# Kernel tuning notes

Measured on AMD Instinct MI355X. Metric: run time of the kernel, lower is better.

## Reference

```python
import jax, jax.numpy as jnp
import numpy as np

N, C, T, V = 64, 64, 64, 25   # batch, channels, frames, joints
S, W = 8, 3                   # num_subset, window_size
IC = C // S                   # inter_channels = out_channels // num_subset = 8
OC = 64                       # out_channels
EPS = 1e-5


def setup_inputs() -> dict:
    key = jax.random.key(0)
    ks = jax.random.split(key, 24)
    std = 0.05
    x = jax.random.normal(ks[0], (N, C, V, T), jnp.float32)
    # fixed skeleton graphs (buffers, non-trainable)
    graph = (jax.random.uniform(ks[1], (S, V, V)) > 0.7).astype(jnp.float32)
    graph = jnp.clip(graph + jnp.eye(V, dtype=jnp.float32)[None], 0.0, 1.0)
    graph_a = jax.random.uniform(ks[2], (V, V), jnp.float32) / V
    # conv1x1 weights (out, in) + biases
    in_w = jax.random.normal(ks[3], (S * IC, C), jnp.float32) * std
    in_b = jax.random.normal(ks[4], (S * IC,), jnp.float32) * 0.01
    inup_w = jax.random.normal(ks[5], (S * IC, C), jnp.float32) * std
    inup_b = jax.random.normal(ks[6], (S * IC,), jnp.float32) * 0.01
    diff_w = jax.random.normal(ks[7], (C, C), jnp.float32) * std
    diff_b = jax.random.normal(ks[8], (C,), jnp.float32) * 0.01
    att0 = jnp.ones((1, S, W * V, V), jnp.float32) / V  # attention0s
    out_w = jax.random.normal(ks[9], (OC, S * C), jnp.float32) * std
    out_b = jax.random.normal(ks[10], (OC,), jnp.float32) * 0.01
    out_gamma = jnp.ones((OC,), jnp.float32)
    out_beta = jnp.zeros((OC,), jnp.float32)
    out_rm = jax.random.normal(ks[11], (OC,), jnp.float32) * 0.01
    out_rv = jnp.ones((OC,), jnp.float32)
    ff_w = jax.random.normal(ks[12], (OC, OC), jnp.float32) * std
    ff_b = jax.random.normal(ks[13], (OC,), jnp.float32) * 0.01
    ff_gamma = jnp.ones((OC,), jnp.float32)
    ff_beta = jnp.zeros((OC,), jnp.float32)
    ff_rm = jax.random.normal(ks[14], (OC,), jnp.float32) * 0.01
    ff_rv = jnp.ones((OC,), jnp.float32)
    return dict(x=x, graph=graph, graph_a=graph_a, in_w=in_w, in_b=in_b,
                inup_w=inup_w, inup_b=inup_b, diff_w=diff_w, diff_b=diff_b,
                att0=att0, out_w=out_w, out_b=out_b, out_gamma=out_gamma,
                out_beta=out_beta, out_rm=out_rm, out_rv=out_rv, ff_w=ff_w,
                ff_b=ff_b, ff_gamma=ff_gamma, ff_beta=ff_beta, ff_rm=ff_rm,
                ff_rv=ff_rv)


def _bn(x, g, b, m, v):  # inference-mode BatchNorm2d over channel dim 1
    scale = (g / jnp.sqrt(v + EPS))[None, :, None, None]
    return x * scale + (b - m * g / jnp.sqrt(v + EPS))[None, :, None, None]


def _leaky(x):
    return jnp.where(x > 0, x, 0.1 * x)


def _forward(x, graph, graph_a, in_w, in_b, inup_w, inup_b, diff_w, diff_b,
             att0, out_w, out_b, out_gamma, out_beta, out_rm, out_rv,
             ff_w, ff_b, ff_gamma, ff_beta, ff_rm, ff_rv):
    xp = jnp.transpose(x, (0, 1, 3, 2))          # (N,C,T,V)
    identity = xp
    # temporal window unfold: (N,C,T,W*V)
    xpad = jnp.pad(xp, ((0, 0), (0, 0), (1, 1), (0, 0)))
    upf = jnp.stack([xpad[:, :, w:w + T, :] for w in range(W)], axis=3)
    upf = upf.reshape(N, C, T, W * V)
    # q/k projections (conv1x1)
    k = (jnp.einsum('nctv,oc->notv', xp, in_w) + in_b[None, :, None, None])
    k = k.reshape(N, S, IC, T, V)
    q = (jnp.einsum('nctu,oc->notu', upf, inup_w) + inup_b[None, :, None, None])
    q = q.reshape(N, S, IC, T, W * V)
    att = jnp.einsum('nsctu,nsctv->nsuv', q, k) / (IC * T)  # (N,S,WV,V)
    # per-subset adjacency mask (graph[i] tiled over window rows)
    mask = jnp.tile(graph, (1, W, 1)) > 0                    # (S,WV,V)
    att = jnp.where(mask[None], att, jnp.float32(-9e15))
    att = jax.nn.softmax(att, axis=-1)
    # diff gate
    d = jnp.einsum('nctu,uv->nctv', xp, graph_a)
    d = jnp.einsum('nctv,oc->notv', d, diff_w) + diff_b[None, :, None, None]
    d = jnp.tile(d, (1, 1, 1, W)) - upf                      # (N,C,T,WV)
    d = d.reshape(N, S, C // S, T, W, V)
    gate = jax.nn.sigmoid(d.mean(axis=(2, 3, 5)))            # (N,S,W)
    att = att * jnp.tile(gate[..., None], (1, 1, V, 1))      # (N,S,WV,1) tiled
    att = att + att0
    # aggregate
    y = jnp.einsum('nctu,nsuv->nsctv', upf, att).reshape(N, S * C, T, V)
    y = _bn(jnp.einsum('nctv,oc->notv', y, out_w) + out_b[None, :, None, None],
            out_gamma, out_beta, out_rm, out_rv)
    y = _leaky(xp + y)                                       # downs1 = identity
    y = _bn(jnp.einsum('nctv,oc->notv', y, ff_w) + ff_b[None, :, None, None],
            ff_gamma, ff_beta, ff_rm, ff_rv)
    y = _leaky(xp + y)                                       # downs2 = identity
    z = jax.nn.relu(y + identity)
    return jnp.transpose(z, (0, 1, 3, 2))                    # back to (N,C,V,T)


def reference(x, graph, graph_a, in_w, in_b, inup_w, inup_b, diff_w, diff_b,
              att0, out_w, out_b, out_gamma, out_beta, out_rm, out_rv,
              ff_w, ff_b, ff_gamma, ff_beta, ff_rm, ff_rv):
    return _forward(x, graph, graph_a, in_w, in_b, inup_w, inup_b, diff_w,
                    diff_b, att0, out_w, out_b, out_gamma, out_beta, out_rm,
                    out_rv, ff_w, ff_b, ff_gamma, ff_beta, ff_rm, ff_rv)
```

## Files before the change

### kernel.cpp

```cpp
#include <hip/hip_runtime.h>
#include <hip/hip_bf16.h>
#include <math.h>

#define Nn 64
#define Cn 64
#define Tn 64
#define Vn 25
#define Sn 8
#define ICn 8
#define Wn 3
#define WVn 75

typedef __attribute__((ext_vector_type(8))) short s16x8;
typedef __attribute__((ext_vector_type(4))) short s16x4;
typedef __attribute__((ext_vector_type(4))) float f32x4;

#define MFMA16(a, b, c) __builtin_amdgcn_mfma_f32_16x16x32_bf16(a, b, c, 0, 0, 0)

static __device__ inline unsigned short f2bf(float f) {
    __hip_bfloat16 h = __float2bfloat16(f);
    return *reinterpret_cast<unsigned short*>(&h);
}
static __device__ inline float bf2f(unsigned short u) {
    union { unsigned int i; float f; } x;
    x.i = ((unsigned int)u) << 16;
    return x.f;
}

__global__ __launch_bounds__(64) void k_red(const float* __restrict__ x,
                                            const float* __restrict__ ga,
                                            const float* __restrict__ ow,
                                            const float* __restrict__ fw,
                                            float* __restrict__ red,
                                            unsigned short* __restrict__ owb,
                                            unsigned short* __restrict__ fwb) {
    const int c = blockIdx.x, n = blockIdx.y;
    const int lane = threadIdx.x;
    if (n == 0) {
        for (int j8 = 0; j8 < 8; ++j8) {
            const int q = c * 512 + j8 * 64 + lane;
            const int j = q & 7, ln = (q >> 3) & 63, fi = q >> 9;
            const int wvq = fi >> 4, ksq = fi & 15;
            owb[q] = f2bf(ow[(wvq * 16 + (ln & 15)) * 512 + ksq * 32 + (ln >> 4) * 8 + j]);
        }
        {
            const int q = c * 64 + lane;
            const int j = q & 7, ln = (q >> 3) & 63, fi = q >> 9;
            const int wvq = fi >> 1, ksq = fi & 1;
            fwb[q] = f2bf(fw[(wvq * 16 + (ln & 15)) * 64 + ksq * 32 + (ln >> 4) * 8 + j]);
        }
    }
    float rs = 0.f, r0 = 0.f, r63 = 0.f, xg = 0.f;
    if (lane < Vn) {
        const float* row = x + ((size_t)(n * Cn + c) * Vn + lane) * Tn;
        float g = 0.f;
        for (int j = 0; j < Vn; ++j) g += ga[lane * Vn + j];
        for (int t = 0; t < Tn; ++t) rs += row[t];
        r0 = row[0];
        r63 = row[Tn - 1];
        xg = rs * g;
    }
    for (int off = 32; off > 0; off >>= 1) {
        rs += __shfl_down(rs, off);
        r0 += __shfl_down(r0, off);
        r63 += __shfl_down(r63, off);
        xg += __shfl_down(xg, off);
    }
    if (lane == 0) {
        float* p = red + (size_t)(n * Cn + c) * 4;
        p[0] = rs; p[1] = r0; p[2] = r63; p[3] = xg;
    }
}

__global__ __launch_bounds__(256) void k_proj2(
    const float* __restrict__ x,
    const float* __restrict__ in_w, const float* __restrict__ in_b,
    const float* __restrict__ inup_w, const float* __restrict__ inup_b,
    unsigned short* __restrict__ pk, unsigned short* __restrict__ pq) {
    const int n = blockIdx.x, v = blockIdx.y;
    const int tid = threadIdx.x;
    const int lane = tid & 63, wv = tid >> 6;
    const int r16 = lane & 15, g4 = lane >> 4;

    __shared__ unsigned short WL[128 * 64];
    __shared__ unsigned short XT[64 * 64];
    __shared__ unsigned short CL[64 * 128];
    __shared__ float bias[128];

    if (tid < 128) bias[tid] = (tid < 64) ? in_b[tid] : inup_b[tid - 64];

    for (int idx = tid; idx < 2048; idx += 256) {
        const int o2 = idx >> 4, c4 = idx & 15;
        const float4 d = (o2 < 64)
            ? *(const float4*)(in_w + o2 * 64 + c4 * 4)
            : *(const float4*)(inup_w + (o2 - 64) * 64 + c4 * 4);
        s16x4 p;
        p[0] = (short)f2bf(d.x); p[1] = (short)f2bf(d.y);
        p[2] = (short)f2bf(d.z); p[3] = (short)f2bf(d.w);
        const int ch = c4 >> 1;
        *(s16x4*)&WL[o2 * 64 + (((ch ^ (o2 & 7))) << 3) + (c4 & 1) * 4] = p;
    }
    for (int idx = tid; idx < 1024; idx += 256) {
        const int c = idx >> 4, t4 = idx & 15;
        const float4 d = *(const float4*)(x +
            ((size_t)((n * Cn + c) * Vn + v)) * Tn + t4 * 4);
        const float dv[4] = {d.x, d.y, d.z, d.w};
#pragma unroll
        for (int jj = 0; jj < 4; ++jj) {
            const int t = t4 * 4 + jj;
            XT[t * 64 + (((c >> 3) ^ (t & 7)) << 3) + (c & 7)] = f2bf(dv[jj]);
        }
    }
    __syncthreads();

#pragma unroll
    for (int mi = 0; mi < 2; ++mi) {
        const int mt = wv * 2 + mi;
        const int o2r = mt * 16 + r16;
#pragma unroll
        for (int nt2 = 0; nt2 < 4; ++nt2) {
            const int t = nt2 * 16 + r16;
            f32x4 acc = (f32x4){0.f, 0.f, 0.f, 0.f};
#pragma unroll
            for (int ks = 0; ks < 2; ++ks) {
                const int ch = ks * 4 + g4;
                const s16x8 a = *(const s16x8*)&WL[o2r * 64 + ((ch ^ (o2r & 7)) << 3)];
                const s16x8 b = *(const s16x8*)&XT[t * 64 + ((ch ^ (t & 7)) << 3)];
                acc = MFMA16(a, b, acc);
            }
            const int tcol = nt2 * 16 + r16;
            const int ob = mt * 16 + g4 * 4;
            s16x4 p;
#pragma unroll
            for (int r = 0; r < 4; ++r) p[r] = f2bf(acc[r] + bias[ob + r]);
            const int ch = ob >> 3;
            *(s16x4*)&CL[tcol * 128 + ((ch ^ (tcol & 7)) << 3) + (ob & 7)] = p;
        }
    }
    __syncthreads();

    for (int jj = tid; jj < 1024; jj += 256) {
        const int t = jj & 63, p = jj >> 6;
        const s16x8 d = *(const s16x8*)&CL[t * 128 + ((p ^ (t & 7)) << 3)];
        const int s8 = p & 7;
        unsigned short* dst = (p < 8) ? pk : pq;
        *(s16x8*)(dst + ((((size_t)(n * Sn + s8) * Vn + v) * Tn + t) << 3)) = d;
    }
}

__global__ __launch_bounds__(256) void k_att3(
    const unsigned short* __restrict__ pq, const unsigned short* __restrict__ pk,
    const float* __restrict__ inup_b, const float* __restrict__ graph,
    const float* __restrict__ att0, const float* __restrict__ red,
    const float* __restrict__ diff_w, const float* __restrict__ diff_b,
    unsigned short* __restrict__ attB) {
    const int n = blockIdx.x, s = blockIdx.y;
    const int tid = threadIdx.x;
    const int lane = tid & 63, wv = tid >> 6;
    const int r16 = lane & 15, g4 = lane >> 4;

    __shared__ unsigned short QS[25 * 536];
    __shared__ unsigned short KS[32 * 512];
    __shared__ float attL[80 * 33];
    __shared__ float gp4[8][4];
    __shared__ float g3[3];

    if (tid < 8) {
        const int oc = s * ICn + tid;
        float a = 0.f;
        for (int c = 0; c < Cn; ++c)
            a += red[(n * Cn + c) * 4 + 3] * diff_w[oc * Cn + c];
        gp4[tid][0] = a + 1600.f * diff_b[oc];
        gp4[tid][1] = red[(n * Cn + oc) * 4 + 0];
        gp4[tid][2] = red[(n * Cn + oc) * 4 + 1];
        gp4[tid][3] = red[(n * Cn + oc) * 4 + 2];
    }
    for (int i = tid; i < 2048; i += 256) {
        const int t = i & 63, v = i >> 6;
        s16x8 d = (s16x8){0, 0, 0, 0, 0, 0, 0, 0};
        if (v < Vn)
            d = *(const s16x8*)(pk + ((((size_t)(n * Sn + s) * Vn + v) * Tn + t) << 3));
        *(s16x8*)&KS[v * 512 + ((t ^ (v & 7)) << 3)] = d;
    }
    for (int i = tid; i < 1600; i += 256) {
        const int t = i & 63, uu = i >> 6;
        const s16x8 d = *(const s16x8*)(pq +
            ((((size_t)(n * Sn + s) * Vn + uu) * Tn + t) << 3));
        *(s16x8*)&QS[uu * 536 + (t + 1) * 8] = d;
    }
    if (tid < 50) {
        const int uu = tid >> 1, slot = (tid & 1) * 65;
#pragma unroll
        for (int cc = 0; cc < ICn; ++cc)
            QS[uu * 536 + slot * 8 + cc] = f2bf(inup_b[s * ICn + cc]);
    }
    __syncthreads();

    for (int tile = wv; tile < 10; tile += 4) {
        const int mt = tile >> 1, nt = tile & 1;
        const int u = mt * 16 + r16;
        const int w = u / 25, uu = u % 25;
        const int v = nt * 16 + r16;
        const unsigned short* qbase = &QS[uu * 536 + (g4 + w) * 8];
        const unsigned short* kbase = &KS[v * 512];
        f32x4 acc = (f32x4){0.f, 0.f, 0.f, 0.f};
#pragma unroll
        for (int kb = 0; kb < 16; ++kb) {
            const s16x8 af = *(const s16x8*)(qbase + kb * 32);
            const s16x8 bf = *(const s16x8*)(kbase + (((kb * 4 + g4) ^ (v & 7)) << 3));
            acc = MFMA16(af, bf, acc);
        }
#pragma unroll
        for (int r = 0; r < 4; ++r)
            attL[(mt * 16 + g4 * 4 + r) * 33 + v] = acc[r];
    }
    if (tid == 0) {
        float sumd2 = 0.f, rsum = 0.f, rr0 = 0.f, rr63 = 0.f;
#pragma unroll
        for (int cc = 0; cc < 8; ++cc) {
            sumd2 += gp4[cc][0]; rsum += gp4[cc][1];
            rr0 += gp4[cc][2]; rr63 += gp4[cc][3];
        }
        const float inv = 1.f / 12800.f;
        g3[0] = 1.f / (1.f + expf(-(sumd2 - (rsum - rr63)) * inv));
        g3[1] = 1.f / (1.f + expf(-(sumd2 - rsum) * inv));
        g3[2] = 1.f / (1.f + expf(-(sumd2 - (rsum - rr0)) * inv));
    }
    __syncthreads();

    if (tid < WVn) {
        const int u = tid, u0 = u % Vn;
        const float* gr = graph + (s * Vn + u0) * Vn;
        float av[Vn];
        float mx = -1e30f;
#pragma unroll
        for (int v = 0; v < Vn; ++v) {
            float a = attL[u * 33 + v] * (1.f / 512.f);
            av[v] = (gr[v] > 0.f) ? a : -1e30f;
            mx = fmaxf(mx, av[v]);
        }
        float ssum = 0.f;
#pragma unroll
        for (int v = 0; v < Vn; ++v) {
            float e = (av[v] > -1e29f) ? expf(av[v] - mx) : 0.f;
            av[v] = e;
            ssum += e;
        }
        const float sc = g3[u % Wn] / ssum;
        const float* a0 = att0 + (s * WVn + u) * Vn;
#pragma unroll
        for (int v = 0; v < Vn; ++v) attL[u * 33 + v] = av[v] * sc + a0[v];
    }
    __syncthreads();

    unsigned short* ab = attB + ((size_t)(n * Sn + s)) * 3072;
    for (int idx = tid; idx < 3072; idx += 256) {
        const int j = idx & 7, ln = (idx >> 3) & 63, f = idx >> 9;
        const int k = f >> 1, nt = f & 1;
        const int v = nt * 16 + (ln & 15);
        const int vp = (ln >> 4) * 8 + j;
        float val = (v < Vn && vp < Vn) ? attL[(k * Vn + vp) * 33 + v] : 0.f;
        ab[idx] = f2bf(val);
    }
}

__global__ __launch_bounds__(256) void k_trans(const float* __restrict__ x,
                                               unsigned short* __restrict__ xT) {
    const int n = blockIdx.x, cb = blockIdx.y;
    const int c0 = cb * 4;
    const int tid = threadIdx.x;
    __shared__ unsigned short XL[4][25][66];

    for (int i = tid; i < 1600; i += 256) {
        const int piece = i & 15, row = i >> 4;
        const int cl = row / 25, v = row - cl * 25;
        const float4 d = *(const float4*)(x +
            ((size_t)((n * Cn + c0 + cl) * Vn + v)) * Tn + piece * 4);
        unsigned short* dst = &XL[cl][v][piece * 4];
        dst[0] = f2bf(d.x); dst[1] = f2bf(d.y); dst[2] = f2bf(d.z); dst[3] = f2bf(d.w);
    }
    __syncthreads();
    for (int j = tid; j < 1024; j += 256) {
        const int p = j & 3, cl = (j >> 2) & 3, t = j >> 4;
        const int v0 = (p ^ cl) * 8;
        unsigned short buf[8];
#pragma unroll
        for (int jj = 0; jj < 8; ++jj) {
            const int v = v0 + jj;
            buf[jj] = (v < Vn) ? XL[cl][v][t] : (unsigned short)0;
        }
        *(s16x8*)(xT + ((size_t)(n * Tn + t) * 2048) + (c0 + cl) * 32 + p * 8) =
            *(const s16x8*)buf;
    }
}

__global__ __launch_bounds__(256, 3) void k_main11(
    const unsigned short* __restrict__ xT, const unsigned short* __restrict__ attB,
    const unsigned short* __restrict__ out_wbf, const float* __restrict__ out_b,
    const float* __restrict__ og, const float* __restrict__ obeta,
    const float* __restrict__ orm, const float* __restrict__ orv,
    const unsigned short* __restrict__ ff_wbf, const float* __restrict__ ff_b,
    const float* __restrict__ fg, const float* __restrict__ fbeta,
    const float* __restrict__ frm, const float* __restrict__ frv,
    float* __restrict__ out) {
    const int n = blockIdx.x, t = blockIdx.y;
    const int tid = threadIdx.x;
    const int lane = tid & 63, wv = tid >> 6;
    const int r16 = lane & 15, g4 = lane >> 4;

    __shared__ unsigned short xs3[3 * 2048];
    __shared__ unsigned short y2L[32 * 512];
    __shared__ unsigned short y1L[32 * 64];
    __shared__ float bnp[384];

    if (tid < 64) {
        int o = tid;
        float so = og[o] * rsqrtf(orv[o] + 1e-5f);
        bnp[o] = so; bnp[64 + o] = obeta[o] - orm[o] * so; bnp[128 + o] = out_b[o];
        float sf = fg[o] * rsqrtf(frv[o] + 1e-5f);
        bnp[192 + o] = sf; bnp[256 + o] = fbeta[o] - frm[o] * sf; bnp[320 + o] = ff_b[o];
    }
    for (int ch = tid; ch < 768; ch += 256) {
        const int kb = ch >> 8, off = ch & 255;
        const int tg = t - 1 + kb;
        s16x8 d = (s16x8){0, 0, 0, 0, 0, 0, 0, 0};
        if (tg >= 0 && tg < Tn)
            d = *(const s16x8*)(xT + ((size_t)(n * Tn + tg) * 2048) + off * 8);
        *(s16x8*)&xs3[ch * 8] = d;
    }
    __syncthreads();

    s16x8 af[4][3];
#pragma unroll
    for (int m = 0; m < 4; ++m) {
        const int c = m * 16 + r16;
#pragma unroll
        for (int kb = 0; kb < 3; ++kb)
            af[m][kb] = *(const s16x8*)&xs3[kb * 2048 + c * 32 + ((g4 ^ (c & 3)) << 3)];
    }
#pragma unroll
    for (int si = 0; si < 2; ++si) {
        const int s = wv * 2 + si;
        const unsigned short* aB = attB + ((size_t)(n * Sn + s)) * 3072;
        s16x8 bfr[3][2];
#pragma unroll
        for (int k = 0; k < 3; ++k)
#pragma unroll
            for (int nt = 0; nt < 2; ++nt)
                bfr[k][nt] = *(const s16x8*)(aB + (((k * 2 + nt) * 64 + lane) << 3));
#pragma unroll
        for (int m = 0; m < 4; ++m) {
            f32x4 c0 = (f32x4){0.f, 0.f, 0.f, 0.f};
            f32x4 c1 = (f32x4){0.f, 0.f, 0.f, 0.f};
#pragma unroll
            for (int kb = 0; kb < 3; ++kb) {
                c0 = MFMA16(af[m][kb], bfr[kb][0], c0);
                c1 = MFMA16(af[m][kb], bfr[kb][1], c1);
            }
            const int cw = m * 16 + g4 * 4;
            s16x4 p0, p1;
#pragma unroll
            for (int r = 0; r < 4; ++r) { p0[r] = f2bf(c0[r]); p1[r] = f2bf(c1[r]); }
            const int v0 = r16, v1 = 16 + r16;
            *(s16x4*)&y2L[v0 * 512 + (s * 8 + ((cw >> 3) ^ (v0 & 7))) * 8 + (cw & 7)] = p0;
            *(s16x4*)&y2L[v1 * 512 + (s * 8 + ((cw >> 3) ^ (v1 & 7))) * 8 + (cw & 7)] = p1;
        }
    }
    __syncthreads();

    f32x4 accO[2];
    accO[0] = (f32x4){0.f, 0.f, 0.f, 0.f};
    accO[1] = (f32x4){0.f, 0.f, 0.f, 0.f};
#pragma unroll
    for (int ks = 0; ks < 16; ++ks) {
        const s16x8 wa = *(const s16x8*)(out_wbf +
            ((((size_t)(wv * 16 + ks)) * 64 + lane) << 3));
        const int cidx = ks * 4 + g4;
        const int srow = cidx >> 3, lc = cidx & 7;
#pragma unroll
        for (int na = 0; na < 2; ++na) {
            const int v = na * 16 + r16;
            const s16x8 b = *(const s16x8*)&y2L[v * 512 + (srow * 8 + (lc ^ (v & 7))) * 8];
            accO[na] = MFMA16(wa, b, accO[na]);
        }
    }
    float xvc[2][4];
    const int ob = wv * 16 + g4 * 4;
#pragma unroll
    for (int na = 0; na < 2; ++na) {
        const int v = na * 16 + r16;
        s16x4 p;
#pragma unroll
        for (int r = 0; r < 4; ++r) {
            const int o = ob + r;
            const float xv = bf2f(xs3[2048 + o * 32 + ((((v >> 3)) ^ (o & 3)) << 3) + (v & 7)]);
            xvc[na][r] = xv;
            float val = (accO[na][r] + bnp[128 + o]) * bnp[o] + bnp[64 + o];
            float y1 = xv + val;
            y1 = (y1 > 0.f) ? y1 : 0.1f * y1;
            p[r] = f2bf(y1);
        }
        *(s16x4*)&y1L[v * 64 + (((ob >> 3) ^ (v & 7)) << 3) + (ob & 7)] = p;
    }
    __syncthreads();

    f32x4 accF[2];
    accF[0] = (f32x4){0.f, 0.f, 0.f, 0.f};
    accF[1] = (f32x4){0.f, 0.f, 0.f, 0.f};
#pragma unroll
    for (int ks = 0; ks < 2; ++ks) {
        const s16x8 fa = *(const s16x8*)(ff_wbf + (((wv * 2 + ks) * 64 + lane) << 3));
        const int cidx = ks * 4 + g4;
#pragma unroll
        for (int na = 0; na < 2; ++na) {
            const int v = na * 16 + r16;
            const s16x8 b = *(const s16x8*)&y1L[v * 64 + ((cidx ^ (v & 7)) << 3)];
            accF[na] = MFMA16(fa, b, accF[na]);
        }
    }
#pragma unroll
    for (int na = 0; na < 2; ++na) {
        const int v = na * 16 + r16;
        if (v < Vn) {
#pragma unroll
            for (int r = 0; r < 4; ++r) {
                const int o = ob + r;
                const float xv = xvc[na][r];
                float val = (accF[na][r] + bnp[320 + o]) * bnp[192 + o] + bnp[256 + o];
                float y2v = xv + val;
                y2v = (y2v > 0.f) ? y2v : 0.1f * y2v;
                float outv = y2v + xv;
                outv = (outv > 0.f) ? outv : 0.f;
                out[((size_t)(n * Cn + o) * Vn + v) * Tn + t] = outv;
            }
        }
    }
}

extern "C" void kernel_launch(void* const* d_in, const int* in_sizes, int n_in,
                              void* d_out, int out_size, void* d_ws, size_t ws_size,
                              hipStream_t stream) {
    const float* x       = (const float*)d_in[0];
    const float* graph   = (const float*)d_in[1];
    const float* graph_a = (const float*)d_in[2];
    const float* in_w    = (const float*)d_in[3];
    const float* in_b    = (const float*)d_in[4];
    const float* inup_w  = (const float*)d_in[5];
    const float* inup_b  = (const float*)d_in[6];
    const float* diff_w  = (const float*)d_in[7];
    const float* diff_b  = (const float*)d_in[8];
    const float* att0    = (const float*)d_in[9];
    const float* out_w   = (const float*)d_in[10];
    const float* out_b   = (const float*)d_in[11];
    const float* og      = (const float*)d_in[12];
    const float* obeta   = (const float*)d_in[13];
    const float* orm     = (const float*)d_in[14];
    const float* orv     = (const float*)d_in[15];
    const float* ff_w    = (const float*)d_in[16];
    const float* ff_b    = (const float*)d_in[17];
    const float* fg      = (const float*)d_in[18];
    const float* fbeta   = (const float*)d_in[19];
    const float* frm     = (const float*)d_in[20];
    const float* frv     = (const float*)d_in[21];
    float* out = (float*)d_out;

    char* wsb = (char*)d_ws;
    float* red_ws  = (float*)(wsb);
    unsigned short* attB = (unsigned short*)(wsb + 71680);
    unsigned short* owb  = (unsigned short*)(wsb + 3217408);
    unsigned short* fwb  = (unsigned short*)(wsb + 3282944);
    unsigned short* pq = (unsigned short*)(wsb + 3291136);
    unsigned short* pk = (unsigned short*)(wsb + 16398336);
    unsigned short* xT = (unsigned short*)(wsb + 3291136);

    k_red<<<dim3(Cn, Nn), 64, 0, stream>>>(x, graph_a, out_w, ff_w, red_ws, owb, fwb);
    k_proj2<<<dim3(Nn, Vn), 256, 0, stream>>>(x, in_w, in_b, inup_w, inup_b, pk, pq);
    k_att3<<<dim3(Nn, Sn), 256, 0, stream>>>(pq, pk, inup_b, graph, att0,
                                             red_ws, diff_w, diff_b, attB);
    k_trans<<<dim3(Nn, 16), 256, 0, stream>>>(x, xT);
    k_main11<<<dim3(Nn, Tn), 256, 0, stream>>>(xT, attB, owb, out_b, og, obeta,
                                               orm, orv, fwb, ff_b, fg, fbeta,
                                               frm, frv, out);
}
```

Before: 107.7 us.

## Coalesce main output via staging buffer and restructure reduction kernel per batch

```diff
diff --git a/kernel.cpp b/kernel.cpp
--- a/kernel.cpp
+++ b/kernel.cpp
@@ -27,48 +27,59 @@
     return x.f;
 }
 
-__global__ __launch_bounds__(64) void k_red(const float* __restrict__ x,
-                                            const float* __restrict__ ga,
-                                            const float* __restrict__ ow,
-                                            const float* __restrict__ fw,
-                                            float* __restrict__ red,
-                                            unsigned short* __restrict__ owb,
-                                            unsigned short* __restrict__ fwb) {
-    const int c = blockIdx.x, n = blockIdx.y;
-    const int lane = threadIdx.x;
+__global__ __launch_bounds__(256) void k_red3(const float* __restrict__ x,
+                                              const float* __restrict__ ga,
+                                              const float* __restrict__ ow,
+                                              const float* __restrict__ fw,
+                                              float* __restrict__ red,
+                                              unsigned short* __restrict__ owb,
+                                              unsigned short* __restrict__ fwb) {
+    const int n = blockIdx.x;
+    const int tid = threadIdx.x;
+    __shared__ float rsL[1600], r0L[1600], r63L[1600], garow[32];
+
     if (n == 0) {
-        for (int j8 = 0; j8 < 8; ++j8) {
-            const int q = c * 512 + j8 * 64 + lane;
+        for (int q = tid; q < 32768; q += 256) {
             const int j = q & 7, ln = (q >> 3) & 63, fi = q >> 9;
             const int wvq = fi >> 4, ksq = fi & 15;
             owb[q] = f2bf(ow[(wvq * 16 + (ln & 15)) * 512 + ksq * 32 + (ln >> 4) * 8 + j]);
         }
-        {
-            const int q = c * 64 + lane;
+        for (int q = tid; q < 4096; q += 256) {
             const int j = q & 7, ln = (q >> 3) & 63, fi = q >> 9;
             const int wvq = fi >> 1, ksq = fi & 1;
             fwb[q] = f2bf(fw[(wvq * 16 + (ln & 15)) * 64 + ksq * 32 + (ln >> 4) * 8 + j]);
         }
     }
-    float rs = 0.f, r0 = 0.f, r63 = 0.f, xg = 0.f;
-    if (lane < Vn) {
-        const float* row = x + ((size_t)(n * Cn + c) * Vn + lane) * Tn;
+    if (tid >= 192 && tid < 192 + Vn) {
+        const int v = tid - 192;
         float g = 0.f;
-        for (int j = 0; j < Vn; ++j) g += ga[lane * Vn + j];
-        for (int t = 0; t < Tn; ++t) rs += row[t];
-        r0 = row[0];
-        r63 = row[Tn - 1];
-        xg = rs * g;
-    }
-    for (int off = 32; off > 0; off >>= 1) {
-        rs += __shfl_down(rs, off);
-        r0 += __shfl_down(r0, off);
-        r63 += __shfl_down(r63, off);
-        xg += __shfl_down(xg, off);
-    }
-    if (lane == 0) {
-        float* p = red + (size_t)(n * Cn + c) * 4;
-        p[0] = rs; p[1] = r0; p[2] = r63; p[3] = xg;
+        for (int j = 0; j < Vn; ++j) g += ga[v * Vn + j];
+        garow[v] = g;
+    }
+    const float* xn = x + (size_t)n * Cn * Vn * Tn;
+    for (int i = 0; i < 100; ++i) {
+        const int idx = tid + i * 256;
+        const int row = idx >> 4, t4 = idx & 15;
+        const float4 d = *(const float4*)(xn + (size_t)row * Tn + t4 * 4);
+        float s = d.x + d.y + d.z + d.w;
+#pragma unroll
+        for (int off = 8; off > 0; off >>= 1) s += __shfl_down(s, off, 16);
+        if (t4 == 0)  { rsL[row] = s; r0L[row] = d.x; }
+        if (t4 == 15) { r63L[row] = d.w; }
+    }
+    __syncthreads();
+    if (tid < Cn) {
+        const int c = tid;
+        float rs = 0.f, r0 = 0.f, r63 = 0.f, xg = 0.f;
+        for (int v = 0; v < Vn; ++v) {
+            const float rv = rsL[c * Vn + v];
+            rs += rv;
+            r0 += r0L[c * Vn + v];
+            r63 += r63L[c * Vn + v];
+            xg += rv * garow[v];
+        }
+        float4 p; p.x = rs; p.y = r0; p.z = r63; p.w = xg;
+        *(float4*)(red + (size_t)(n * Cn + c) * 4) = p;
     }
 }
 
@@ -294,6 +305,155 @@
     }
 }
 
+template <int STORE_T>
+static __device__ void main_core(
+    const unsigned short* __restrict__ xT, const unsigned short* __restrict__ attB,
+    const unsigned short* __restrict__ out_wbf, const float* __restrict__ out_b,
+    const float* __restrict__ og, const float* __restrict__ obeta,
+    const float* __restrict__ orm, const float* __restrict__ orv,
+    const unsigned short* __restrict__ ff_wbf, const float* __restrict__ ff_b,
+    const float* __restrict__ fg, const float* __restrict__ fbeta,
+    const float* __restrict__ frm, const float* __restrict__ frv,
+    float* __restrict__ out, float* __restrict__ outT) {
+    const int n = blockIdx.x, t = blockIdx.y;
+    const int tid = threadIdx.x;
+    const int lane = tid & 63, wv = tid >> 6;
+    const int r16 = lane & 15, g4 = lane >> 4;
+
+    __shared__ unsigned short xs3[3 * 2048];
+    __shared__ unsigned short y2L[32 * 512];
+    __shared__ unsigned short y1L[32 * 64];
+    __shared__ float bnp[384];
+
+    if (tid < 64) {
+        int o = tid;
+        float so = og[o] * rsqrtf(orv[o] + 1e-5f);
+        bnp[o] = so; bnp[64 + o] = obeta[o] - orm[o] * so; bnp[128 + o] = out_b[o];
+        float sf = fg[o] * rsqrtf(frv[o] + 1e-5f);
+        bnp[192 + o] = sf; bnp[256 + o] = fbeta[o] - frm[o] * sf; bnp[320 + o] = ff_b[o];
+    }
+    for (int ch = tid; ch < 768; ch += 256) {
+        const int kb = ch >> 8, off = ch & 255;
+        const int tg = t - 1 + kb;
+        s16x8 d = (s16x8){0, 0, 0, 0, 0, 0, 0, 0};
+        if (tg >= 0 && tg < Tn)
+            d = *(const s16x8*)(xT + ((size_t)(n * Tn + tg) * 2048) + off * 8);
+        *(s16x8*)&xs3[ch * 8] = d;
+    }
+    __syncthreads();
+
+    s16x8 af[4][3];
+#pragma unroll
+    for (int m = 0; m < 4; ++m) {
+        const int c = m * 16 + r16;
+#pragma unroll
+        for (int kb = 0; kb < 3; ++kb)
+            af[m][kb] = *(const s16x8*)&xs3[kb * 2048 + c * 32 + ((g4 ^ (c & 3)) << 3)];
+    }
+#pragma unroll
+    for (int si = 0; si < 2; ++si) {
+        const int s = wv * 2 + si;
+        const unsigned short* aB = attB + ((size_t)(n * Sn + s)) * 3072;
+        s16x8 bfr[3][2];
+#pragma unroll
+        for (int k = 0; k < 3; ++k)
+#pragma unroll
+            for (int nt = 0; nt < 2; ++nt)
+                bfr[k][nt] = *(const s16x8*)(aB + (((k * 2 + nt) * 64 + lane) << 3));
+#pragma unroll
+        for (int m = 0; m < 4; ++m) {
+            f32x4 c0 = (f32x4){0.f, 0.f, 0.f, 0.f};
+            f32x4 c1 = (f32x4){0.f, 0.f, 0.f, 0.f};
+#pragma unroll
+            for (int kb = 0; kb < 3; ++kb) {
+                c0 = MFMA16(af[m][kb], bfr[kb][0], c0);
+                c1 = MFMA16(af[m][kb], bfr[kb][1], c1);
+            }
+            const int cw = m * 16 + g4 * 4;
+            s16x4 p0, p1;
+#pragma unroll
+            for (int r = 0; r < 4; ++r) { p0[r] = f2bf(c0[r]); p1[r] = f2bf(c1[r]); }
+            const int v0 = r16, v1 = 16 + r16;
+            *(s16x4*)&y2L[v0 * 512 + (s * 8 + ((cw >> 3) ^ (v0 & 7))) * 8 + (cw & 7)] = p0;
+            *(s16x4*)&y2L[v1 * 512 + (s * 8 + ((cw >> 3) ^ (v1 & 7))) * 8 + (cw & 7)] = p1;
+        }
+    }
+    __syncthreads();
+
+    f32x4 accO[2];
+    accO[0] = (f32x4){0.f, 0.f, 0.f, 0.f};
+    accO[1] = (f32x4){0.f, 0.f, 0.f, 0.f};
+#pragma unroll
+    for (int ks = 0; ks < 16; ++ks) {
+        const s16x8 wa = *(const s16x8*)(out_wbf +
+            ((((size_t)(wv * 16 + ks)) * 64 + lane) << 3));
+        const int cidx = ks * 4 + g4;
+        const int srow = cidx >> 3, lc = cidx & 7;
+#pragma unroll
+        for (int na = 0; na < 2; ++na) {
+            const int v = na * 16 + r16;
+            const s16x8 b = *(const s16x8*)&y2L[v * 512 + (srow * 8 + (lc ^ (v & 7))) * 8];
+            accO[na] = MFMA16(wa, b, accO[na]);
+        }
+    }
+    float xvc[2][4];
+    const int ob = wv * 16 + g4 * 4;
+#pragma unroll
+    for (int na = 0; na < 2; ++na) {
+        const int v = na * 16 + r16;
+        s16x4 p;
+#pragma unroll
+        for (int r = 0; r < 4; ++r) {
+            const int o = ob + r;
+            const float xv = bf2f(xs3[2048 + o * 32 + ((((v >> 3)) ^ (o & 3)) << 3) + (v & 7)]);
+            xvc[na][r] = xv;
+            float val = (accO[na][r] + bnp[128 + o]) * bnp[o] + bnp[64 + o];
+            float y1 = xv + val;
+            y1 = (y1 > 0.f) ? y1 : 0.1f * y1;
+            p[r] = f2bf(y1);
+        }
+        *(s16x4*)&y1L[v * 64 + (((ob >> 3) ^ (v & 7)) << 3) + (ob & 7)] = p;
+    }
+    __syncthreads();
+
+    f32x4 accF[2];
+    accF[0] = (f32x4){0.f, 0.f, 0.f, 0.f};
+    accF[1] = (f32x4){0.f, 0.f, 0.f, 0.f};
+#pragma unroll
+    for (int ks = 0; ks < 2; ++ks) {
+        const s16x8 fa = *(const s16x8*)(ff_wbf + (((wv * 2 + ks) * 64 + lane) << 3));
+        const int cidx = ks * 4 + g4;
+#pragma unroll
+        for (int na = 0; na < 2; ++na) {
+            const int v = na * 16 + r16;
+            const s16x8 b = *(const s16x8*)&y1L[v * 64 + ((cidx ^ (v & 7)) << 3)];
+            accF[na] = MFMA16(fa, b, accF[na]);
+        }
+    }
+#pragma unroll
+    for (int na = 0; na < 2; ++na) {
+        const int v = na * 16 + r16;
+        if (v < Vn) {
+            float4 pv;
+            float* pvp = (float*)&pv;
+#pragma unroll
+            for (int r = 0; r < 4; ++r) {
+                const int o = ob + r;
+                const float xv = xvc[na][r];
+                float val = (accF[na][r] + bnp[320 + o]) * bnp[192 + o] + bnp[256 + o];
+                float y2v = xv + val;
+                y2v = (y2v > 0.f) ? y2v : 0.1f * y2v;
+                float outv = y2v + xv;
+                outv = (outv > 0.f) ? outv : 0.f;
+                if (STORE_T) pvp[r] = outv;
+                else out[((size_t)(n * Cn + o) * Vn + v) * Tn + t] = outv;
+            }
+            if (STORE_T)
+                *(float4*)(outT + ((size_t)(n * Tn + t) * Vn + v) * 64 + ob) = pv;
+        }
+    }
+}
+
 __global__ __launch_bounds__(256, 3) void k_main11(
     const unsigned short* __restrict__ xT, const unsigned short* __restrict__ attB,
     const unsigned short* __restrict__ out_wbf, const float* __restrict__ out_b,
@@ -303,137 +463,45 @@
     const float* __restrict__ fg, const float* __restrict__ fbeta,
     const float* __restrict__ frm, const float* __restrict__ frv,
     float* __restrict__ out) {
-    const int n = blockIdx.x, t = blockIdx.y;
+    main_core<0>(xT, attB, out_wbf, out_b, og, obeta, orm, orv, ff_wbf, ff_b,
+                 fg, fbeta, frm, frv, out, nullptr);
+}
+
+__global__ __launch_bounds__(256, 3) void k_main12(
+    const unsigned short* __restrict__ xT, const unsigned short* __restrict__ attB,
+    const unsigned short* __restrict__ out_wbf, const float* __restrict__ out_b,
+    const float* __restrict__ og, const float* __restrict__ obeta,
+    const float* __restrict__ orm, const float* __restrict__ orv,
+    const unsigned short* __restrict__ ff_wbf, const float* __restrict__ ff_b,
+    const float* __restrict__ fg, const float* __restrict__ fbeta,
+    const float* __restrict__ frm, const float* __restrict__ frv,
+    float* __restrict__ outT) {
+    main_core<1>(xT, attB, out_wbf, out_b, og, obeta, orm, orv, ff_wbf, ff_b,
+                 fg, fbeta, frm, frv, nullptr, outT);
+}
+
+__global__ __launch_bounds__(256) void k_out(const float* __restrict__ outT,
+                                             float* __restrict__ out) {
+    const int n = blockIdx.x, tc = blockIdx.y;
+    const int t0 = tc * 4;
     const int tid = threadIdx.x;
-    const int lane = tid & 63, wv = tid >> 6;
-    const int r16 = lane & 15, g4 = lane >> 4;
-
-    __shared__ unsigned short xs3[3 * 2048];
-    __shared__ unsigned short y2L[32 * 512];
-    __shared__ unsigned short y1L[32 * 64];
-    __shared__ float bnp[384];
-
-    if (tid < 64) {
-        int o = tid;
-        float so = og[o] * rsqrtf(orv[o] + 1e-5f);
-        bnp[o] = so; bnp[64 + o] = obeta[o] - orm[o] * so; bnp[128 + o] = out_b[o];
-        float sf = fg[o] * rsqrtf(frv[o] + 1e-5f);
-        bnp[192 + o] = sf; bnp[256 + o] = fbeta[o] - frm[o] * sf; bnp[320 + o] = ff_b[o];
-    }
-    for (int ch = tid; ch < 768; ch += 256) {
-        const int kb = ch >> 8, off = ch & 255;
-        const int tg = t - 1 + kb;
-        s16x8 d = (s16x8){0, 0, 0, 0, 0, 0, 0, 0};
-        if (tg >= 0 && tg < Tn)
-            d = *(const s16x8*)(xT + ((size_t)(n * Tn + tg) * 2048) + off * 8);
-        *(s16x8*)&xs3[ch * 8] = d;
-    }
-    __syncthreads();
-
-    s16x8 af[4][3];
-#pragma unroll
-    for (int m = 0; m < 4; ++m) {
-        const int c = m * 16 + r16;
-#pragma unroll
-        for (int kb = 0; kb < 3; ++kb)
-            af[m][kb] = *(const s16x8*)&xs3[kb * 2048 + c * 32 + ((g4 ^ (c & 3)) << 3)];
-    }
-#pragma unroll
-    for (int si = 0; si < 2; ++si) {
-        const int s = wv * 2 + si;
-        const unsigned short* aB = attB + ((size_t)(n * Sn + s)) * 3072;
-        s16x8 bfr[3][2];
-#pragma unroll
-        for (int k = 0; k < 3; ++k)
-#pragma unroll
-            for (int nt = 0; nt < 2; ++nt)
-                bfr[k][nt] = *(const s16x8*)(aB + (((k * 2 + nt) * 64 + lane) << 3));
-#pragma unroll
-        for (int m = 0; m < 4; ++m) {
-            f32x4 c0 = (f32x4){0.f, 0.f, 0.f, 0.f};
-            f32x4 c1 = (f32x4){0.f, 0.f, 0.f, 0.f};
-#pragma unroll
-            for (int kb = 0; kb < 3; ++kb) {
-                c0 = MFMA16(af[m][kb], bfr[kb][0], c0);
-                c1 = MFMA16(af[m][kb], bfr[kb][1], c1);
-            }
-            const int cw = m * 16 + g4 * 4;
-            s16x4 p0, p1;
-#pragma unroll
-            for (int r = 0; r < 4; ++r) { p0[r] = f2bf(c0[r]); p1[r] = f2bf(c1[r]); }
-            const int v0 = r16, v1 = 16 + r16;
-            *(s16x4*)&y2L[v0 * 512 + (s * 8 + ((cw >> 3) ^ (v0 & 7))) * 8 + (cw & 7)] = p0;
-            *(s16x4*)&y2L[v1 * 512 + (s * 8 + ((cw >> 3) ^ (v1 & 7))) * 8 + (cw & 7)] = p1;
-        }
-    }
-    __syncthreads();
-
-    f32x4 accO[2];
-    accO[0] = (f32x4){0.f, 0.f, 0.f, 0.f};
-    accO[1] = (f32x4){0.f, 0.f, 0.f, 0.f};
-#pragma unroll
-    for (int ks = 0; ks < 16; ++ks) {
-        const s16x8 wa = *(const s16x8*)(out_wbf +
-            ((((size_t)(wv * 16 + ks)) * 64 + lane) << 3));
-        const int cidx = ks * 4 + g4;
-        const int srow = cidx >> 3, lc = cidx & 7;
-#pragma unroll
-        for (int na = 0; na < 2; ++na) {
-            const int v = na * 16 + r16;
-            const s16x8 b = *(const s16x8*)&y2L[v * 512 + (srow * 8 + (lc ^ (v & 7))) * 8];
-            accO[na] = MFMA16(wa, b, accO[na]);
-        }
-    }
-    float xvc[2][4];
-    const int ob = wv * 16 + g4 * 4;
-#pragma unroll
-    for (int na = 0; na < 2; ++na) {
-        const int v = na * 16 + r16;
-        s16x4 p;
-#pragma unroll
-        for (int r = 0; r < 4; ++r) {
-            const int o = ob + r;
-            const float xv = bf2f(xs3[2048 + o * 32 + ((((v >> 3)) ^ (o & 3)) << 3) + (v & 7)]);
-            xvc[na][r] = xv;
-            float val = (accO[na][r] + bnp[128 + o]) * bnp[o] + bnp[64 + o];
-            float y1 = xv + val;
-            y1 = (y1 > 0.f) ? y1 : 0.1f * y1;
-            p[r] = f2bf(y1);
-        }
-        *(s16x4*)&y1L[v * 64 + (((ob >> 3) ^ (v & 7)) << 3) + (ob & 7)] = p;
-    }
-    __syncthreads();
-
-    f32x4 accF[2];
-    accF[0] = (f32x4){0.f, 0.f, 0.f, 0.f};
-    accF[1] = (f32x4){0.f, 0.f, 0.f, 0.f};
-#pragma unroll
-    for (int ks = 0; ks < 2; ++ks) {
-        const s16x8 fa = *(const s16x8*)(ff_wbf + (((wv * 2 + ks) * 64 + lane) << 3));
-        const int cidx = ks * 4 + g4;
-#pragma unroll
-        for (int na = 0; na < 2; ++na) {
-            const int v = na * 16 + r16;
-            const s16x8 b = *(const s16x8*)&y1L[v * 64 + ((cidx ^ (v & 7)) << 3)];
-            accF[na] = MFMA16(fa, b, accF[na]);
-        }
-    }
-#pragma unroll
-    for (int na = 0; na < 2; ++na) {
-        const int v = na * 16 + r16;
-        if (v < Vn) {
-#pragma unroll
-            for (int r = 0; r < 4; ++r) {
-                const int o = ob + r;
-                const float xv = xvc[na][r];
-                float val = (accF[na][r] + bnp[320 + o]) * bnp[192 + o] + bnp[256 + o];
-                float y2v = xv + val;
-                y2v = (y2v > 0.f) ? y2v : 0.1f * y2v;
-                float outv = y2v + xv;
-                outv = (outv > 0.f) ? outv : 0.f;
-                out[((size_t)(n * Cn + o) * Vn + v) * Tn + t] = outv;
-            }
-        }
+    __shared__ float outL[4 * 1600];
+
+#pragma unroll
+    for (int tl = 0; tl < 4; ++tl) {
+        const float* src = outT + ((size_t)(n * Tn + t0 + tl) * Vn) * 64;
+        for (int i = tid; i < 1600; i += 256)
+            outL[tl * 1600 + i] = src[i];
+    }
+    __syncthreads();
+    for (int r = tid; r < 1600; r += 256) {
+        const int v = r >> 6, o = r & 63;
+        float4 pv;
+        pv.x = outL[0 * 1600 + r];
+        pv.y = outL[1 * 1600 + r];
+        pv.z = outL[2 * 1600 + r];
+        pv.w = outL[3 * 1600 + r];
+        *(float4*)(out + ((size_t)(n * Cn + o) * Vn + v) * Tn + t0) = pv;
     }
 }
 
@@ -472,13 +540,22 @@
     unsigned short* pq = (unsigned short*)(wsb + 3291136);
     unsigned short* pk = (unsigned short*)(wsb + 16398336);
     unsigned short* xT = (unsigned short*)(wsb + 3291136);
-
-    k_red<<<dim3(Cn, Nn), 64, 0, stream>>>(x, graph_a, out_w, ff_w, red_ws, owb, fwb);
+    float* outT = (float*)(wsb + 20068352);
+    const bool big = ws_size >= (size_t)46282752;
+
+    k_red3<<<dim3(Nn), 256, 0, stream>>>(x, graph_a, out_w, ff_w, red_ws, owb, fwb);
     k_proj2<<<dim3(Nn, Vn), 256, 0, stream>>>(x, in_w, in_b, inup_w, inup_b, pk, pq);
     k_att3<<<dim3(Nn, Sn), 256, 0, stream>>>(pq, pk, inup_b, graph, att0,
                                              red_ws, diff_w, diff_b, attB);
     k_trans<<<dim3(Nn, 16), 256, 0, stream>>>(x, xT);
-    k_main11<<<dim3(Nn, Tn), 256, 0, stream>>>(xT, attB, owb, out_b, og, obeta,
-                                               orm, orv, fwb, ff_b, fg, fbeta,
-                                               frm, frv, out);
-}
+    if (big) {
+        k_main12<<<dim3(Nn, Tn), 256, 0, stream>>>(xT, attB, owb, out_b, og, obeta,
+                                                   orm, orv, fwb, ff_b, fg, fbeta,
+                                                   frm, frv, outT);
+        k_out<<<dim3(Nn, Tn / 4), 256, 0, stream>>>(outT, out);
+    } else {
+        k_main11<<<dim3(Nn, Tn), 256, 0, stream>>>(xT, attB, owb, out_b, og, obeta,
+                                                   orm, orv, fwb, ff_b, fg, fbeta,
+                                                   frm, frv, out);
+    }
+}
```

After: 165.5 us. 53.7% more time.
